# Kernel tuning notes

Measured on AMD Instinct MI355X. Metric: run time of the kernel, lower is better.

## Reference

```python
import jax, jax.numpy as jnp
import numpy as np

B, S, H = 2, 1024, 2048
E, F = 16, 1024          # num_experts, moe_intermediate_size
TOP_K = 4
SH_F = 5632              # shared_expert_intermediate_size


def setup_inputs() -> dict:
    key = jax.random.key(0)
    ks = jax.random.split(key, 9)
    sc = 0.02
    return {
        'hidden_states': jax.random.normal(ks[0], (B, S, H), dtype=jnp.float32),
        'w_router': jax.random.normal(ks[1], (H, E), dtype=jnp.float32) * sc,
        'w_gate': jax.random.normal(ks[2], (E, H, F), dtype=jnp.float32) * sc,
        'w_up': jax.random.normal(ks[3], (E, H, F), dtype=jnp.float32) * sc,
        'w_down': jax.random.normal(ks[4], (E, F, H), dtype=jnp.float32) * sc,
        'w_sh_gate': jax.random.normal(ks[5], (H, SH_F), dtype=jnp.float32) * sc,
        'w_sh_up': jax.random.normal(ks[6], (H, SH_F), dtype=jnp.float32) * sc,
        'w_sh_down': jax.random.normal(ks[7], (SH_F, H), dtype=jnp.float32) * sc,
        'w_sh_expert_gate': jax.random.normal(ks[8], (H, 1), dtype=jnp.float32) * sc,
    }


def reference(hidden_states, w_router, w_gate, w_up, w_down,
              w_sh_gate, w_sh_up, w_sh_down, w_sh_expert_gate):
    b, s, h = hidden_states.shape
    x = hidden_states.reshape(-1, h)                      # [T, H]

    # router: softmax over all experts, then top-k, renormalize (norm_topk_prob=True)
    router_logits = x @ w_router                          # [T, E]
    probs = jax.nn.softmax(router_logits, axis=-1)
    topk_w, topk_ids = jax.lax.top_k(probs, TOP_K)        # [T, k]
    topk_w = topk_w / jnp.sum(topk_w, axis=-1, keepdims=True)

    # combine matrix [T, E]: routing weight per (token, expert)
    combine = jnp.sum(
        jax.nn.one_hot(topk_ids, E, dtype=x.dtype) * topk_w[..., None], axis=1)

    # experts: SwiGLU per expert, weighted-combined before down projection
    g = jnp.einsum('th,ehf->tef', x, w_gate)              # [T, E, F]
    u = jnp.einsum('th,ehf->tef', x, w_up)
    act = jax.nn.silu(g) * u                              # SiluAndMul
    act = act * combine[:, :, None]                       # fold routing weights
    moe_out = jnp.einsum('tef,efh->th', act, w_down)      # [T, H]

    # shared expert with sigmoid gate
    sg = jax.nn.silu(x @ w_sh_gate) * (x @ w_sh_up)       # [T, SH_F]
    shared = sg @ w_sh_down                               # [T, H]
    gate = jax.nn.sigmoid(x @ w_sh_expert_gate)           # [T, 1]
    out = moe_out + gate * shared
    return out.reshape(b, s, h)
```

## Files before the change

### kernel.cpp

```cpp
#include <hip/hip_runtime.h>
#include <hip/hip_bf16.h>
#include <stdint.h>

#define T_TOK 2048
#define HD    2048
#define NE    16
#define FF    1024
#define TOPK  4
#define SHF   5632

typedef __attribute__((ext_vector_type(8))) short short8;
typedef __attribute__((ext_vector_type(4))) float f32x4;

typedef const __attribute__((address_space(1))) uint32_t* gp1_t;
typedef __attribute__((address_space(3))) uint32_t* lp3_t;

__device__ __forceinline__ void gload_lds16(const void* g, void* l) {
  __builtin_amdgcn_global_load_lds((gp1_t)g, (lp3_t)l, 16, 0, 0);
}

__device__ __forceinline__ unsigned short f2bf(float f) {
  __hip_bfloat16 h = __float2bfloat16(f);
  return __builtin_bit_cast(unsigned short, h);
}
__device__ __forceinline__ float bf2f(unsigned short u) {
  return __uint_as_float(((uint32_t)u) << 16);
}

__global__ __launch_bounds__(256) void k_prep(const float* __restrict__ x,
                                              unsigned short* __restrict__ xb, int n) {
  int i = blockIdx.x * blockDim.x + threadIdx.x;
  int stride = gridDim.x * blockDim.x;
  for (; i < n; i += stride) xb[i] = f2bf(x[i]);
}

__global__ __launch_bounds__(256) void k_transpose(const float* __restrict__ src,
    unsigned short* __restrict__ dst, int K, int N) {
  __shared__ unsigned short tile[64][72];
  const int k0 = blockIdx.x * 64;
  const int n0 = blockIdx.y * 64;
  const size_t boff = (size_t)blockIdx.z * K * N;
  src += boff; dst += boff;
  const int t = threadIdx.x;
  const int c4 = (t & 15) * 4;
  const int kr0 = (t >> 4) * 4;
#pragma unroll
  for (int j = 0; j < 4; ++j) {
    int kr = kr0 + j;
    float4 v = *(const float4*)(src + (size_t)(k0 + kr) * N + n0 + c4);
    tile[c4 + 0][kr] = f2bf(v.x);
    tile[c4 + 1][kr] = f2bf(v.y);
    tile[c4 + 2][kr] = f2bf(v.z);
    tile[c4 + 3][kr] = f2bf(v.w);
  }
  __syncthreads();
  const int nr = t >> 2;
  const int kc = (t & 3) * 8;
  unsigned short* orow = dst + (size_t)(n0 + nr) * K + k0;
  *(short8*)(orow + kc)      = *(const short8*)(&tile[nr][kc]);
  *(short8*)(orow + kc + 32) = *(const short8*)(&tile[nr][kc + 32]);
}

__global__ __launch_bounds__(256) void k_router2(
    const float* __restrict__ x, const float* __restrict__ wr,
    const float* __restrict__ wsg,
    int* __restrict__ tk_ids, float* __restrict__ tk_w,
    float* __restrict__ gate_sh) {
  const int t = blockIdx.x * 4 + (threadIdx.x >> 6);
  const int lane = threadIdx.x & 63;
  const float4* x4  = (const float4*)(x + (size_t)t * HD);
  const float4* wg4 = (const float4*)wsg;
  float p[NE + 1];
#pragma unroll
  for (int e = 0; e <= NE; ++e) p[e] = 0.f;
#pragma unroll
  for (int j = 0; j < 8; ++j) {
    const int i4 = lane + 64 * j;
    float4 xv = x4[i4];
    const float4* wrow = (const float4*)(wr + (size_t)i4 * 4 * NE);
#pragma unroll
    for (int r = 0; r < 4; ++r) {
      float xs = (&xv.x)[r];
#pragma unroll
      for (int c = 0; c < 4; ++c) {
        float4 wv = wrow[r * 4 + c];
        p[c * 4 + 0] += xs * wv.x;
        p[c * 4 + 1] += xs * wv.y;
        p[c * 4 + 2] += xs * wv.z;
        p[c * 4 + 3] += xs * wv.w;
      }
    }
    float4 gv = wg4[i4];
    p[NE] += xv.x * gv.x + xv.y * gv.y + xv.z * gv.z + xv.w * gv.w;
  }
#pragma unroll
  for (int e = 0; e <= NE; ++e) {
    float v = p[e];
    for (int off = 32; off; off >>= 1) v += __shfl_xor(v, off);
    p[e] = v;
  }
  if (lane == 0) {
    gate_sh[t] = 1.f / (1.f + __expf(-p[NE]));
    float l[NE];
#pragma unroll
    for (int e = 0; e < NE; ++e) l[e] = p[e];
    int ids[TOPK]; float lg[TOPK];
#pragma unroll
    for (int k = 0; k < TOPK; ++k) {
      int best = 0; float bv = l[0];
#pragma unroll
      for (int e = 1; e < NE; ++e) { if (l[e] > bv) { bv = l[e]; best = e; } }
      ids[k] = best; lg[k] = bv; l[best] = -1e30f;
    }
    float m = lg[0], s = 0.f, w[TOPK];
#pragma unroll
    for (int k = 0; k < TOPK; ++k) { w[k] = __expf(lg[k] - m); s += w[k]; }
    float inv = 1.f / s;
#pragma unroll
    for (int k = 0; k < TOPK; ++k) {
      tk_ids[t * TOPK + k] = ids[k];
      tk_w[t * TOPK + k] = w[k] * inv;
    }
  }
}

__global__ __launch_bounds__(256) void k_offsets2(
    const int* __restrict__ tk_ids, int* __restrict__ counts,
    int* __restrict__ offsets) {
  __shared__ int h[NE];
  const int tid = threadIdx.x;
  if (tid < NE) h[tid] = 0;
  __syncthreads();
  for (int i = tid; i < T_TOK * TOPK; i += 256) atomicAdd(&h[tk_ids[i]], 1);
  __syncthreads();
  if (tid == 0) {
    int off = 0;
    for (int e = 0; e < NE; ++e) { counts[e] = h[e]; offsets[e] = off; off += h[e]; }
    offsets[NE] = off;
  }
}

__global__ __launch_bounds__(256) void k_build(
    const int* __restrict__ tk_ids, const float* __restrict__ tk_w,
    const int* __restrict__ offsets, int* __restrict__ list,
    float* __restrict__ wpair) {
  const int e = blockIdx.x;
  const int tid = threadIdx.x, lane = tid & 63, w = tid >> 6;
  __shared__ int wbase[4];
  __shared__ int sbase;
  if (tid == 0) sbase = 0;
  __syncthreads();
  const int obase = offsets[e];
  for (int c = 0; c < T_TOK / 256; ++c) {
    int t = c * 256 + tid;
    int m = -1;
#pragma unroll
    for (int k = 0; k < TOPK; ++k)
      if (tk_ids[t * TOPK + k] == e) m = k;
    unsigned long long mask = __ballot(m >= 0);
    int posw = __popcll(mask & ((1ull << lane) - 1ull));
    if (lane == 0) wbase[w] = __popcll(mask);
    __syncthreads();
    int wb = 0;
#pragma unroll
    for (int j = 0; j < 4; ++j) if (j < w) wb += wbase[j];
    int tot = wbase[0] + wbase[1] + wbase[2] + wbase[3];
    if (m >= 0) {
      int pos = sbase + wb + posw;
      list[e * T_TOK + pos] = t;
      wpair[obase + pos] = tk_w[t * TOPK + m];
    }
    __syncthreads();
    if (tid == 0) sbase += tot;
    __syncthreads();
  }
}

template<int MODE>
__global__ __launch_bounds__(256) void k_gemm(
    const unsigned short* __restrict__ A, int lda, int K,
    const unsigned short* __restrict__ B0, const unsigned short* __restrict__ B1,
    int nsplit, size_t strideB,
    unsigned short* __restrict__ O0, unsigned short* __restrict__ O1, int ldo,
    float* __restrict__ OF,
    const int* __restrict__ counts, const int* __restrict__ offsets,
    const int* __restrict__ list, const float* __restrict__ gate_sh)
{
  constexpr bool DBUF = (MODE == 1 || MODE == 3);
  __shared__ unsigned short lds[DBUF ? 2 * 16384 : 16384];
  __shared__ int tokLDS[128];

  const int cb = blockIdx.x, rb = blockIdx.y;
  const int e = (MODE <= 1) ? blockIdx.z : 0;
  const int tid = threadIdx.x, l = tid & 63, wid = tid >> 6;
  const int wr = wid >> 1, wc = wid & 1;

  int cnt = T_TOK;
  if (MODE <= 1) {
    cnt = counts[e];
    if (rb * 128 >= cnt) return;
  }
  if (MODE == 0) {
    if (tid < 128) {
      int r = rb * 128 + tid;
      tokLDS[tid] = list[e * T_TOK + (r < cnt ? r : cnt - 1)];
    }
    __syncthreads();
  }

  const int swz8 = ((l & 7) ^ (l >> 3)) * 8;
  const unsigned short* Bsel = (cb < nsplit) ? B0 : B1;
  const int cb2 = (cb < nsplit) ? cb : cb - nsplit;
  const size_t eoff = (MODE <= 1) ? (size_t)e * strideB : (size_t)0;

  const unsigned short* aS[4];
  const unsigned short* bS[4];
#pragma unroll
  for (int i = 0; i < 4; ++i) {
    int rloc = wid * 32 + i * 8 + (l >> 3);
    int arow;
    if (MODE == 0) arow = tokLDS[rloc];
    else if (MODE == 1) { int rr = rb * 128 + rloc; if (rr >= cnt) rr = cnt - 1; arow = offsets[e] + rr; }
    else arow = rb * 128 + rloc;
    aS[i] = A + (size_t)arow * lda + swz8;
    bS[i] = Bsel + eoff + (size_t)(cb2 * 128 + rloc) * K + swz8;
  }

  f32x4 acc[4][4];
#pragma unroll
  for (int mf = 0; mf < 4; ++mf)
#pragma unroll
    for (int nf = 0; nf < 4; ++nf) acc[mf][nf] = (f32x4){0.f, 0.f, 0.f, 0.f};

  const int nkt = K / 64;

  if constexpr (!DBUF) {
    for (int kt = 0; kt < nkt; ++kt) {
      const int k0 = kt * 64;
      unsigned short* base = &lds[0] + (wid * 32) * 64;
#pragma unroll
      for (int i = 0; i < 4; ++i) {
        gload_lds16(aS[i] + k0, base + i * 8 * 64);
        gload_lds16(bS[i] + k0, base + i * 8 * 64 + 8192);
      }
      __syncthreads();
      const char* lAb = (const char*)&lds[0];
      const char* lBb = lAb + 16384;
#pragma unroll
      for (int kk = 0; kk < 2; ++kk) {
        const int kb = kk * 64 + ((l >> 4) * 16);
        short8 af[4], bf[4];
#pragma unroll
        for (int mf = 0; mf < 4; ++mf) {
          int row = wr * 64 + mf * 16 + (l & 15);
          af[mf] = *(const short8*)(lAb + row * 128 + (kb ^ ((row & 7) << 4)));
        }
#pragma unroll
        for (int nf = 0; nf < 4; ++nf) {
          int n = wc * 64 + nf * 16 + (l & 15);
          bf[nf] = *(const short8*)(lBb + n * 128 + (kb ^ ((n & 7) << 4)));
        }
#pragma unroll
        for (int mf = 0; mf < 4; ++mf)
#pragma unroll
          for (int nf = 0; nf < 4; ++nf)
            acc[mf][nf] = __builtin_amdgcn_mfma_f32_16x16x32_bf16(af[mf], bf[nf], acc[mf][nf], 0, 0, 0);
      }
      __syncthreads();
    }
  } else {
    auto STAGE = [&](int kt) {
      unsigned short* base = &lds[0] + (kt & 1) * 16384 + (wid * 32) * 64;
      const int k0 = kt * 64;
#pragma unroll
      for (int i = 0; i < 4; ++i) {
        gload_lds16(aS[i] + k0, base + i * 8 * 64);
        gload_lds16(bS[i] + k0, base + i * 8 * 64 + 8192);
      }
    };
    STAGE(0);
    for (int kt = 0; kt < nkt; ++kt) {
      if (kt + 1 < nkt) {
        STAGE(kt + 1);
        asm volatile("s_waitcnt vmcnt(8)" ::: "memory");
      } else {
        asm volatile("s_waitcnt vmcnt(0)" ::: "memory");
      }
      __builtin_amdgcn_s_barrier();
      asm volatile("" ::: "memory");
      const char* lAb = (const char*)(&lds[0] + (kt & 1) * 16384);
      const char* lBb = lAb + 16384;
#pragma unroll
      for (int kk = 0; kk < 2; ++kk) {
        const int kb = kk * 64 + ((l >> 4) * 16);
        short8 af[4], bf[4];
#pragma unroll
        for (int mf = 0; mf < 4; ++mf) {
          int row = wr * 64 + mf * 16 + (l & 15);
          af[mf] = *(const short8*)(lAb + row * 128 + (kb ^ ((row & 7) << 4)));
        }
#pragma unroll
        for (int nf = 0; nf < 4; ++nf) {
          int n = wc * 64 + nf * 16 + (l & 15);
          bf[nf] = *(const short8*)(lBb + n * 128 + (kb ^ ((n & 7) << 4)));
        }
        __builtin_amdgcn_s_setprio(1);
#pragma unroll
        for (int mf = 0; mf < 4; ++mf)
#pragma unroll
          for (int nf = 0; nf < 4; ++nf)
            acc[mf][nf] = __builtin_amdgcn_mfma_f32_16x16x32_bf16(af[mf], bf[nf], acc[mf][nf], 0, 0, 0);
        __builtin_amdgcn_s_setprio(0);
      }
      asm volatile("" ::: "memory");
      __builtin_amdgcn_s_barrier();
      asm volatile("" ::: "memory");
    }
  }

  const int g4 = (l >> 4) * 4;
  const int cL = l & 15;
  const int colb = cb2 * 128 + wc * 64;

  if constexpr (MODE == 0 || MODE == 2) {
    unsigned short* Out = (cb < nsplit) ? O0 : O1;
    const int obase = (MODE == 0) ? offsets[e] : 0;
#pragma unroll
    for (int mf = 0; mf < 4; ++mf)
#pragma unroll
      for (int r = 0; r < 4; ++r) {
        int rloc = rb * 128 + wr * 64 + mf * 16 + g4 + r;
        if (MODE == 0 && rloc >= cnt) continue;
        size_t orow = (size_t)(obase + rloc) * ldo + colb;
#pragma unroll
        for (int nf = 0; nf < 4; ++nf)
          Out[orow + nf * 16 + cL] = f2bf(acc[mf][nf][r]);
      }
  } else if constexpr (MODE == 1) {
#pragma unroll
    for (int mf = 0; mf < 4; ++mf)
#pragma unroll
      for (int r = 0; r < 4; ++r) {
        int rloc = rb * 128 + wr * 64 + mf * 16 + g4 + r;
        if (rloc < cnt) {
          int tok = list[e * T_TOK + rloc];
          float* dst = OF + (size_t)tok * HD + colb;
#pragma unroll
          for (int nf = 0; nf < 4; ++nf)
            atomicAdd(dst + nf * 16 + cL, acc[mf][nf][r]);
        }
      }
  } else {
#pragma unroll
    for (int mf = 0; mf < 4; ++mf)
#pragma unroll
      for (int r = 0; r < 4; ++r) {
        int t = rb * 128 + wr * 64 + mf * 16 + g4 + r;
        float g = gate_sh[t];
        float* dst = OF + (size_t)t * HD + colb;
#pragma unroll
        for (int nf = 0; nf < 4; ++nf)
          dst[nf * 16 + cL] = g * acc[mf][nf][r];
      }
  }
}

__global__ __launch_bounds__(256) void k_silu(
    const unsigned short* __restrict__ gq, unsigned short* __restrict__ uq,
    const float* __restrict__ wrow, long total)
{
  long i = ((long)blockIdx.x * blockDim.x + threadIdx.x) * 4;
  const long stride = (long)gridDim.x * blockDim.x * 4;
  for (; i < total; i += stride) {
    ushort4 gv = *(const ushort4*)(gq + i);
    ushort4 uv = *(const ushort4*)(uq + i);
    float w = wrow ? wrow[i >> 10] : 1.f;
    float a0 = bf2f(gv.x), a1 = bf2f(gv.y), a2 = bf2f(gv.z), a3 = bf2f(gv.w);
    float b0 = bf2f(uv.x), b1 = bf2f(uv.y), b2 = bf2f(uv.z), b3 = bf2f(uv.w);
    ushort4 o;
    o.x = f2bf(a0 / (1.f + __expf(-a0)) * b0 * w);
    o.y = f2bf(a1 / (1.f + __expf(-a1)) * b1 * w);
    o.z = f2bf(a2 / (1.f + __expf(-a2)) * b2 * w);
    o.w = f2bf(a3 / (1.f + __expf(-a3)) * b3 * w);
    *(ushort4*)(uq + i) = o;
  }
}

extern "C" void kernel_launch(void* const* d_in, const int* in_sizes, int n_in,
                              void* d_out, int out_size, void* d_ws, size_t ws_size,
                              hipStream_t stream) {
  const float* x     = (const float*)d_in[0];
  const float* wrout = (const float*)d_in[1];
  const float* wgate = (const float*)d_in[2];
  const float* wup   = (const float*)d_in[3];
  const float* wdown = (const float*)d_in[4];
  const float* wsg   = (const float*)d_in[5];
  const float* wsu   = (const float*)d_in[6];
  const float* wsd   = (const float*)d_in[7];
  const float* wseg  = (const float*)d_in[8];
  float* out = (float*)d_out;

  char* ws = (char*)d_ws;
  unsigned short* xb = (unsigned short*)ws;
  char* region1 = ws + (size_t)(8u << 20);
  unsigned short* sgg  = (unsigned short*)region1;
  unsigned short* sgu  = (unsigned short*)(region1 + (size_t)23068672);
  unsigned short* actg = (unsigned short*)region1;
  unsigned short* actu = (unsigned short*)(region1 + (size_t)(16u << 20));
  char* p3 = region1 + (size_t)46137344;
  int*   counts  = (int*)p3;
  int*   offsets = (int*)(p3 + 256);
  float* gateS   = (float*)(p3 + 512);
  float* wpair   = (float*)(p3 + 512 + 8192);
  int*   list    = (int*)(p3 + 512 + 8192 + 32768);
  int*   tk_ids  = (int*)(p3 + 512 + 8192 + 32768 + 131072);
  float* tk_w    = (float*)(p3 + 512 + 8192 + 32768 + 131072 + 32768);
  char* p4 = p3 + (size_t)(1u << 20);
  unsigned short* W1 = (unsigned short*)p4;
  unsigned short* W2 = (unsigned short*)(p4 + (size_t)(64u << 20));
  (void)ws_size; (void)in_sizes; (void)n_in; (void)out_size;

  const int n = T_TOK * HD;
  k_prep<<<dim3(2048), dim3(256), 0, stream>>>(x, xb, n);
  k_router2<<<dim3(T_TOK / 4), dim3(256), 0, stream>>>(x, wrout, wseg, tk_ids, tk_w, gateS);
  k_offsets2<<<dim3(1), dim3(256), 0, stream>>>(tk_ids, counts, offsets);
  k_build<<<dim3(NE), dim3(256), 0, stream>>>(tk_ids, tk_w, offsets, list, wpair);

  unsigned short* WsgT = W2;
  unsigned short* WsuT = W2 + (size_t)SHF * HD;
  k_transpose<<<dim3(32, 88, 1), dim3(256), 0, stream>>>(wsg, WsgT, HD, SHF);
  k_transpose<<<dim3(32, 88, 1), dim3(256), 0, stream>>>(wsu, WsuT, HD, SHF);

  k_gemm<2><<<dim3(88, 16, 1), dim3(256), 0, stream>>>(
      xb, HD, HD, WsgT, WsuT, 44, (size_t)0,
      sgg, sgu, SHF, (float*)nullptr, counts, offsets, list, (const float*)nullptr);
  k_silu<<<dim3(4096), dim3(256), 0, stream>>>(sgg, sgu, (const float*)nullptr, (long)T_TOK * SHF);

  k_transpose<<<dim3(88, 32, 1), dim3(256), 0, stream>>>(wsd, W1, SHF, HD);
  k_gemm<3><<<dim3(16, 16, 1), dim3(256), 0, stream>>>(
      sgu, SHF, SHF, W1, W1, 1 << 30, (size_t)0,
      (unsigned short*)nullptr, (unsigned short*)nullptr, HD,
      out, counts, offsets, list, gateS);

  k_transpose<<<dim3(32, 16, 16), dim3(256), 0, stream>>>(wgate, W1, HD, FF);
  k_transpose<<<dim3(32, 16, 16), dim3(256), 0, stream>>>(wup,   W2, HD, FF);

  k_gemm<0><<<dim3(16, 16, 16), dim3(256), 0, stream>>>(
      xb, HD, HD, W1, W2, 8, (size_t)HD * FF,
      actg, actu, FF, (float*)nullptr, counts, offsets, list, (const float*)nullptr);
  k_silu<<<dim3(4096), dim3(256), 0, stream>>>(actg, actu, wpair, (long)T_TOK * TOPK * FF);

  k_transpose<<<dim3(16, 32, 16), dim3(256), 0, stream>>>(wdown, W1, FF, HD);
  k_gemm<1><<<dim3(16, 16, 16), dim3(256), 0, stream>>>(
      actu, FF, FF, W1, W1, 1 << 30, (size_t)FF * HD,
      (unsigned short*)nullptr, (unsigned short*)nullptr, HD,
      out, counts, offsets, list, (const float*)nullptr);
}
```

Before: 595.2 us.

## Fuse fp32 weight load and bf16 conversion into single-buffered GEMM modes

For the shared gate/up and routed expert gate/up GEMMs, the kernel now reads the original fp32 weights straight from global memory, converts them to bf16 in registers, and writes them transposed into swizzled LDS, using a new swizzle pattern. Four separate transpose kernels and their round trip of bf16 copies through memory go away. In exchange the B operand is loaded with plain vector loads instead of async global-to-LDS loads, with conversion work in the main loop. Each expert's weights are also re-converted by every row block, which repeats the conversion work.

```diff
diff --git a/kernel.cpp b/kernel.cpp
--- a/kernel.cpp
+++ b/kernel.cpp
@@ -180,6 +180,7 @@
 __global__ __launch_bounds__(256) void k_gemm(
     const unsigned short* __restrict__ A, int lda, int K,
     const unsigned short* __restrict__ B0, const unsigned short* __restrict__ B1,
+    const float* __restrict__ BF0, const float* __restrict__ BF1, int ldbn,
     int nsplit, size_t strideB,
     unsigned short* __restrict__ O0, unsigned short* __restrict__ O1, int ldo,
     float* __restrict__ OF,
@@ -209,9 +210,7 @@
   }
 
   const int swz8 = ((l & 7) ^ (l >> 3)) * 8;
-  const unsigned short* Bsel = (cb < nsplit) ? B0 : B1;
   const int cb2 = (cb < nsplit) ? cb : cb - nsplit;
-  const size_t eoff = (MODE <= 1) ? (size_t)e * strideB : (size_t)0;
 
   const unsigned short* aS[4];
   const unsigned short* bS[4];
@@ -223,7 +222,20 @@
     else if (MODE == 1) { int rr = rb * 128 + rloc; if (rr >= cnt) rr = cnt - 1; arow = offsets[e] + rr; }
     else arow = rb * 128 + rloc;
     aS[i] = A + (size_t)arow * lda + swz8;
-    bS[i] = Bsel + eoff + (size_t)(cb2 * 128 + rloc) * K + swz8;
+    if (DBUF) {
+      const unsigned short* Bsel = (cb < nsplit) ? B0 : B1;
+      const size_t eoff = (MODE == 1) ? (size_t)e * strideB : (size_t)0;
+      bS[i] = Bsel + eoff + (size_t)(cb2 * 128 + rloc) * K + swz8;
+    }
+  }
+
+  const float* bFp = nullptr;
+  const int bn0 = (tid & 31) * 4;
+  const int bk0 = (tid >> 5) * 4;
+  if (!DBUF) {
+    const float* Bsel = (cb < nsplit) ? BF0 : BF1;
+    const size_t eoff = (MODE == 0) ? (size_t)e * strideB : (size_t)0;
+    bFp = Bsel + eoff + cb2 * 128 + bn0;
   }
 
   f32x4 acc[4][4];
@@ -237,11 +249,31 @@
   if constexpr (!DBUF) {
     for (int kt = 0; kt < nkt; ++kt) {
       const int k0 = kt * 64;
-      unsigned short* base = &lds[0] + (wid * 32) * 64;
-#pragma unroll
-      for (int i = 0; i < 4; ++i) {
-        gload_lds16(aS[i] + k0, base + i * 8 * 64);
-        gload_lds16(bS[i] + k0, base + i * 8 * 64 + 8192);
+      unsigned short* baseA = &lds[0] + (wid * 32) * 64;
+#pragma unroll
+      for (int i = 0; i < 4; ++i)
+        gload_lds16(aS[i] + k0, baseA + i * 8 * 64);
+
+      float4 v[2][4];
+#pragma unroll
+      for (int b = 0; b < 2; ++b)
+#pragma unroll
+        for (int j = 0; j < 4; ++j)
+          v[b][j] = *(const float4*)(bFp + (size_t)(k0 + bk0 + b * 32 + j) * ldbn);
+      char* lBc = (char*)(&lds[0]) + 16384;
+#pragma unroll
+      for (int b = 0; b < 2; ++b) {
+        const int kq = bk0 + b * 32;
+        const int chunk = (kq >> 3) << 4;
+        const int sub = (kq & 7) * 2;
+#pragma unroll
+        for (int c = 0; c < 4; ++c) {
+          const int n = bn0 + c;
+          uint32_t lo = (uint32_t)f2bf((&v[b][0].x)[c]) | ((uint32_t)f2bf((&v[b][1].x)[c]) << 16);
+          uint32_t hi = (uint32_t)f2bf((&v[b][2].x)[c]) | ((uint32_t)f2bf((&v[b][3].x)[c]) << 16);
+          const int swzB = ((n & 7) ^ ((n >> 2) & 7)) << 4;
+          *(uint2*)(lBc + n * 128 + (chunk ^ swzB) + sub) = make_uint2(lo, hi);
+        }
       }
       __syncthreads();
       const char* lAb = (const char*)&lds[0];
@@ -258,7 +290,8 @@
 #pragma unroll
         for (int nf = 0; nf < 4; ++nf) {
           int n = wc * 64 + nf * 16 + (l & 15);
-          bf[nf] = *(const short8*)(lBb + n * 128 + (kb ^ ((n & 7) << 4)));
+          const int swzB = ((n & 7) ^ ((n >> 2) & 7)) << 4;
+          bf[nf] = *(const short8*)(lBb + n * 128 + (kb ^ swzB));
         }
 #pragma unroll
         for (int mf = 0; mf < 4; ++mf)
@@ -417,7 +450,6 @@
   float* tk_w    = (float*)(p3 + 512 + 8192 + 32768 + 131072 + 32768);
   char* p4 = p3 + (size_t)(1u << 20);
   unsigned short* W1 = (unsigned short*)p4;
-  unsigned short* W2 = (unsigned short*)(p4 + (size_t)(64u << 20));
   (void)ws_size; (void)in_sizes; (void)n_in; (void)out_size;
 
   const int n = T_TOK * HD;
@@ -426,33 +458,29 @@
   k_offsets2<<<dim3(1), dim3(256), 0, stream>>>(tk_ids, counts, offsets);
   k_build<<<dim3(NE), dim3(256), 0, stream>>>(tk_ids, tk_w, offsets, list, wpair);
 
-  unsigned short* WsgT = W2;
-  unsigned short* WsuT = W2 + (size_t)SHF * HD;
-  k_transpose<<<dim3(32, 88, 1), dim3(256), 0, stream>>>(wsg, WsgT, HD, SHF);
-  k_transpose<<<dim3(32, 88, 1), dim3(256), 0, stream>>>(wsu, WsuT, HD, SHF);
-
   k_gemm<2><<<dim3(88, 16, 1), dim3(256), 0, stream>>>(
-      xb, HD, HD, WsgT, WsuT, 44, (size_t)0,
+      xb, HD, HD, (const unsigned short*)nullptr, (const unsigned short*)nullptr,
+      wsg, wsu, SHF, 44, (size_t)0,
       sgg, sgu, SHF, (float*)nullptr, counts, offsets, list, (const float*)nullptr);
   k_silu<<<dim3(4096), dim3(256), 0, stream>>>(sgg, sgu, (const float*)nullptr, (long)T_TOK * SHF);
 
   k_transpose<<<dim3(88, 32, 1), dim3(256), 0, stream>>>(wsd, W1, SHF, HD);
   k_gemm<3><<<dim3(16, 16, 1), dim3(256), 0, stream>>>(
-      sgu, SHF, SHF, W1, W1, 1 << 30, (size_t)0,
+      sgu, SHF, SHF, W1, W1,
+      (const float*)nullptr, (const float*)nullptr, 0, 1 << 30, (size_t)0,
       (unsigned short*)nullptr, (unsigned short*)nullptr, HD,
       out, counts, offsets, list, gateS);
 
-  k_transpose<<<dim3(32, 16, 16), dim3(256), 0, stream>>>(wgate, W1, HD, FF);
-  k_transpose<<<dim3(32, 16, 16), dim3(256), 0, stream>>>(wup,   W2, HD, FF);
-
   k_gemm<0><<<dim3(16, 16, 16), dim3(256), 0, stream>>>(
-      xb, HD, HD, W1, W2, 8, (size_t)HD * FF,
+      xb, HD, HD, (const unsigned short*)nullptr, (const unsigned short*)nullptr,
+      wgate, wup, FF, 8, (size_t)HD * FF,
       actg, actu, FF, (float*)nullptr, counts, offsets, list, (const float*)nullptr);
   k_silu<<<dim3(4096), dim3(256), 0, stream>>>(actg, actu, wpair, (long)T_TOK * TOPK * FF);
 
   k_transpose<<<dim3(16, 32, 16), dim3(256), 0, stream>>>(wdown, W1, FF, HD);
   k_gemm<1><<<dim3(16, 16, 16), dim3(256), 0, stream>>>(
-      actu, FF, FF, W1, W1, 1 << 30, (size_t)FF * HD,
+      actu, FF, FF, W1, W1,
+      (const float*)nullptr, (const float*)nullptr, 0, 1 << 30, (size_t)FF * HD,
       (unsigned short*)nullptr, (unsigned short*)nullptr, HD,
       out, counts, offsets, list, (const float*)nullptr);
 }
```

New measurement: 612.6 us. 1.03x slower.
